# Optimization experiments

Measured on AMD Instinct MI355X. Metric: run time of the kernel, lower is better.

## Reference

```python
import jax, jax.numpy as jnp
import numpy as np

N = 50000      # num_labels (nodes)
HID = 64       # hidden_dim
HEADS = 4
CH = 16        # hidden_dim // 4 per head
R = 4          # relations
E = 200000     # edges per relation
DEPTH = 2
SLOPE = 0.2    # GATv2 leaky_relu negative slope
EPS = 1e-5     # LayerNorm eps


def layer_norm(x, g, b):
    mu = jnp.mean(x, axis=-1, keepdims=True)
    var = jnp.mean((x - mu) ** 2, axis=-1, keepdims=True)
    return (x - mu) / jnp.sqrt(var + EPS) * g + b


def setup_inputs() -> dict:
    key = jax.random.key(0)
    ks = jax.random.split(key, 8)
    # edges with src != dst (PyG remove_self_loops is then a no-op)
    src = jax.random.randint(ks[0], (R, E), 0, N, dtype=jnp.int32)
    off = jax.random.randint(ks[1], (R, E), 1, N, dtype=jnp.int32)
    dst = ((src + off) % N).astype(jnp.int32)
    edge_index = jnp.stack([src, dst], axis=1)  # [R, 2, E]
    s = 1.0 / np.sqrt(HID)
    return {
        "label_embeddings": jax.random.normal(ks[2], (N, HID), jnp.float32) * 0.5,
        "entry_w": jax.random.normal(ks[3], (HID, HID), jnp.float32) * s,
        "entry_b": jnp.zeros((HID,), jnp.float32),
        "entry_ln_g": jnp.ones((HID,), jnp.float32),
        "entry_ln_b": jnp.zeros((HID,), jnp.float32),
        "conv_wl": jax.random.normal(ks[4], (DEPTH, R, HID, HEADS * CH), jnp.float32) * s,
        "conv_wr": jax.random.normal(ks[5], (DEPTH, R, HID, HEADS * CH), jnp.float32) * s,
        "conv_att": jax.random.normal(ks[6], (DEPTH, R, HEADS, CH), jnp.float32) * (1.0 / np.sqrt(CH)),
        "conv_bias": jnp.zeros((DEPTH, R, HEADS * CH), jnp.float32),
        "norm_g": jnp.ones((HID,), jnp.float32),
        "norm_b": jnp.zeros((HID,), jnp.float32),
        "edge_index": edge_index,
    }


def _gatv2_layer(x, wl, wr, att, bias, src, dst):
    """One GATv2Conv over one relation. x:[N,HID]; returns [N, HEADS*CH]."""
    xl = (x @ wl).reshape(N, HEADS, CH)  # source transform
    xr = (x @ wr).reshape(N, HEADS, CH)  # target transform
    m = xl[src] + xr[dst]                          # [E+N, HEADS, CH]
    e = jnp.einsum('ehc,hc->eh', jax.nn.leaky_relu(m, SLOPE), att)  # [E+N, HEADS]
    # segment softmax over incoming edges of each dst node
    emax = jax.ops.segment_max(e, dst, num_segments=N)  # [N, HEADS]
    a = jnp.exp(e - emax[dst])
    denom = jax.ops.segment_sum(a, dst, num_segments=N)
    alpha = a / denom[dst]                          # every node has a self-loop -> denom > 0
    msg = xl[src] * alpha[..., None]                # [E+N, HEADS, CH]
    out = jax.ops.segment_sum(msg, dst, num_segments=N).reshape(N, HEADS * CH)
    return out + bias


def reference(label_embeddings, entry_w, entry_b, entry_ln_g, entry_ln_b,
              conv_wl, conv_wr, conv_att, conv_bias, norm_g, norm_b, edge_index):
    x = jax.nn.gelu(layer_norm(label_embeddings @ entry_w + entry_b, entry_ln_g, entry_ln_b),
                    approximate=False)
    loop = jnp.arange(N, dtype=edge_index.dtype)
    for layer in range(DEPTH):
        outs = []
        for r in range(R):
            src = jnp.concatenate([edge_index[r, 0], loop])  # add self-loops (PyG default)
            dst = jnp.concatenate([edge_index[r, 1], loop])
            outs.append(_gatv2_layer(x, conv_wl[layer, r], conv_wr[layer, r],
                                     conv_att[layer, r], conv_bias[layer, r], src, dst))
        x = sum(outs) / R                              # HeteroConv aggr='mean'
        x = layer_norm(jax.nn.gelu(x, approximate=False), norm_g, norm_b)  # dropout = identity (eval)
    return x
```

## Files before the change

### kernel.cpp

```cpp
#include <hip/hip_runtime.h>
#include <hip/hip_bf16.h>

#define NN 50000
#define RR 4
#define EE 200000
#define CAP 32

typedef __hip_bfloat16 bf16;
typedef __attribute__((ext_vector_type(8))) short short8;
typedef __attribute__((ext_vector_type(4))) float float4v;
typedef __attribute__((ext_vector_type(2))) float float2v;

__device__ __forceinline__ float b2f(bf16 v) { return __bfloat162float(v); }
__device__ __forceinline__ unsigned short f2bu(float v) {
    bf16 h = __float2bfloat16(v);
    return *(unsigned short*)&h;
}
__device__ __forceinline__ float ldf(const void* p, int i, int isbf) {
    return isbf ? __bfloat162float(((const bf16*)p)[i]) : ((const float*)p)[i];
}
__device__ __forceinline__ int dtype_isbf(const void* lg) {
    return ((const unsigned*)lg)[0] == 0x3F803F80u;
}
__device__ __forceinline__ float gelu_exact(float x) {
    return 0.5f * x * (1.0f + erff(x * 0.70710678118654752f));
}
__device__ __forceinline__ float lrelu(float m) { return fmaxf(m, 0.2f * m); }
__device__ __forceinline__ float2v bp2(unsigned u) {
    float2v f;
    f.x = __uint_as_float(u << 16);
    f.y = __uint_as_float(u & 0xffff0000u);
    return f;
}
__device__ __forceinline__ float2v lrelu2(float2v m) {
    float2v s = m * 0.2f;
    float2v r;
    r.x = fmaxf(m.x, s.x);
    r.y = fmaxf(m.y, s.y);
    return r;
}

#define PW_ENTRY_W 0
#define PW_ENTRY_B 4096
#define PW_LN_G    4160
#define PW_LN_B    4224
#define PW_WL      4288
#define PW_ATT     69824
#define PW_BIAS    70336
#define PW_NG      70848
#define PW_NB      70912
#define PW_TOT     70976

#define WT_ELEMS (2 * RR * 128 * 64)

__global__ __launch_bounds__(256) void cvt_k(const void* ew, const void* eb, const void* lg,
                                             const void* lb, const void* wl, const void* wr,
                                             const void* at, const void* bi, const void* ng,
                                             const void* nb,
                                             float* __restrict__ P, bf16* __restrict__ WT,
                                             int* __restrict__ cnt) {
    int i = blockIdx.x * 256 + threadIdx.x;
    int isbf = dtype_isbf(lg);
    if (i < RR * NN) cnt[i] = 0;
    if (i < WT_ELEMS) {
        int k = i & 63;
        int c = (i >> 6) & 127;
        int lr = i >> 13;
        float v = (c < 64) ? ldf(wl, (lr * 64 + k) * 64 + c, isbf)
                           : ldf(wr, (lr * 64 + k) * 64 + (c - 64), isbf);
        WT[i] = __float2bfloat16(v);
    }
    if (i < PW_TOT) {
        const void* src = nullptr;
        int off = 0;
        if (i < PW_ENTRY_B)      { src = ew; off = i - PW_ENTRY_W; }
        else if (i < PW_LN_G)    { src = eb; off = i - PW_ENTRY_B; }
        else if (i < PW_LN_B)    { src = lg; off = i - PW_LN_G; }
        else if (i < PW_WL)      { src = lb; off = i - PW_LN_B; }
        else if (i < PW_ATT)     { src = nullptr; }
        else if (i < PW_BIAS)    { src = at; off = i - PW_ATT; }
        else if (i < PW_NG)      { src = bi; off = i - PW_BIAS; }
        else if (i < PW_NB)      { src = ng; off = i - PW_NG; }
        else                     { src = nb; off = i - PW_NB; }
        if (src) P[i] = ldf(src, off, isbf);
    }
}

__global__ void scatter_k(const int* __restrict__ ei, int* __restrict__ cnt,
                          int* __restrict__ col) {
    int e = blockIdx.x * 256 + threadIdx.x;
    int r = blockIdx.y;
    if (e < EE) {
        int s = ei[r * 2 * EE + e];
        int d = ei[r * 2 * EE + EE + e];
        int p = atomicAdd(&cnt[r * NN + d], 1);
        if (p < CAP) col[((size_t)r * NN + d) * CAP + p] = s;
    }
}

__global__ __launch_bounds__(256) void entry_k(const void* __restrict__ emb,
                                               const void* __restrict__ lg,
                                               const float* __restrict__ P,
                                               bf16* __restrict__ xout) {
    int wave = (blockIdx.x * 256 + threadIdx.x) >> 6;
    int c = threadIdx.x & 63;
    if (wave >= NN) return;
    int isbf = dtype_isbf(lg);
    float ev = ldf(emb, wave * 64 + c, isbf);
    float acc = 0.f;
#pragma unroll 8
    for (int k = 0; k < 64; k++) {
        float xv = __shfl(ev, k, 64);
        acc += xv * P[PW_ENTRY_W + k * 64 + c];
    }
    acc += P[PW_ENTRY_B + c];
    float s = acc;
#pragma unroll
    for (int m = 1; m < 64; m <<= 1) s += __shfl_xor(s, m, 64);
    float mu = s * (1.f / 64.f);
    float d = acc - mu;
    float vs = d * d;
#pragma unroll
    for (int m = 1; m < 64; m <<= 1) vs += __shfl_xor(vs, m, 64);
    float var = vs * (1.f / 64.f);
    float y = d * rsqrtf(var + 1e-5f) * P[PW_LN_G + c] + P[PW_LN_B + c];
    xout[wave * 64 + c] = __float2bfloat16(gelu_exact(y));
}

__global__ __launch_bounds__(256) void gemm_m(const bf16* __restrict__ X,
                                              const bf16* __restrict__ WTlayer,
                                              bf16* __restrict__ xlB,
                                              bf16* __restrict__ xrB) {
    int r = blockIdx.y;
    const short* Xs = (const short*)X;
    const short* WT = (const short*)(WTlayer + (size_t)r * 8192);
    bf16* xl = xlB + (size_t)r * NN * 64;
    bf16* xr = xrB + (size_t)r * NN * 64;

    __shared__ float sh[16 * 132];
    int t = threadIdx.x;
    int w = t >> 6;
    int lane = t & 63;
    int m = lane & 15, kq = lane >> 4;
    int row0 = blockIdx.x * 16;

    const short* ap = Xs + (row0 + m) * 64 + kq * 8;
    short8 a0 = *(const short8*)ap;
    short8 a1 = *(const short8*)(ap + 32);

#pragma unroll
    for (int tile = 0; tile < 2; tile++) {
        int ct = w * 2 + tile;
        int c0 = ct * 16 + m;
        const short* bp = WT + c0 * 64 + kq * 8;
        short8 b0 = *(const short8*)bp;
        short8 b1 = *(const short8*)(bp + 32);
        float4v acc = {0.f, 0.f, 0.f, 0.f};
        asm volatile(
            "v_mfma_f32_16x16x32_bf16 %0, %1, %2, %0\n\t"
            "v_mfma_f32_16x16x32_bf16 %0, %3, %4, %0\n\t"
            "s_nop 7\n\t"
            "s_nop 7"
            : "+v"(acc)
            : "v"(a0), "v"(b0), "v"(a1), "v"(b1));
#pragma unroll
        for (int i = 0; i < 4; i++) sh[(kq * 4 + i) * 132 + c0] = acc[i];
    }
    __syncthreads();
    int row = t >> 4, cg = (t & 15) * 8;
    float v0 = sh[row * 132 + cg + 0], v1 = sh[row * 132 + cg + 1];
    float v2 = sh[row * 132 + cg + 2], v3 = sh[row * 132 + cg + 3];
    float v4 = sh[row * 132 + cg + 4], v5 = sh[row * 132 + cg + 5];
    float v6 = sh[row * 132 + cg + 6], v7 = sh[row * 132 + cg + 7];
    uint4 u;
    u.x = ((unsigned)f2bu(v1) << 16) | f2bu(v0);
    u.y = ((unsigned)f2bu(v3) << 16) | f2bu(v2);
    u.z = ((unsigned)f2bu(v5) << 16) | f2bu(v4);
    u.w = ((unsigned)f2bu(v7) << 16) | f2bu(v6);
    size_t grow = row0 + row;
    if (cg < 64) *(uint4*)&xl[grow * 64 + cg] = u;
    else         *(uint4*)&xr[grow * 64 + (cg - 64)] = u;
}

__global__ __launch_bounds__(256) void aggfin_k(const bf16* __restrict__ xlB,
                                                const bf16* __restrict__ xrB,
                                                const float* __restrict__ attL,
                                                const float* __restrict__ biasL,
                                                const int* __restrict__ cnt,
                                                const int* __restrict__ col,
                                                const float* __restrict__ P,
                                                const void* __restrict__ lg,
                                                void* __restrict__ outp,
                                                int finalOut) {
    __shared__ float shRes[RR][4][68];
    int t = threadIdx.x;
    int r = t >> 6;
    int lane = t & 63;
    int nodeBase = blockIdx.x * 4;
    int nn = lane >> 4, es = (lane >> 2) & 3, h = lane & 3;
    int node = nodeBase + nn;

    const unsigned* xl = (const unsigned*)(xlB + (size_t)r * NN * 64);
    const unsigned* xr = (const unsigned*)(xrB + (size_t)r * NN * 64);
    const float* att = attL + r * 64;
    const float* bias = biasL + r * 64;

    float2v at2[8], xr2[8];
    {
        const float4* ap = (const float4*)(att + h * 16);
#pragma unroll
        for (int i = 0; i < 4; i++) {
            float4 a = ap[i];
            at2[2 * i].x = a.x * 1.44269504f; at2[2 * i].y = a.y * 1.44269504f;
            at2[2 * i + 1].x = a.z * 1.44269504f; at2[2 * i + 1].y = a.w * 1.44269504f;
        }
        const uint4* q = (const uint4*)(xr + node * 32 + h * 8);
        uint4 u0 = q[0], u1 = q[1];
        xr2[0] = bp2(u0.x); xr2[1] = bp2(u0.y); xr2[2] = bp2(u0.z); xr2[3] = bp2(u0.w);
        xr2[4] = bp2(u1.x); xr2[5] = bp2(u1.y); xr2[6] = bp2(u1.z); xr2[7] = bp2(u1.w);
    }
    int cn = cnt[r * NN + node];
    if (cn > CAP) cn = CAP;
    int total = cn + 1;
    int kmax = total;
    kmax = max(kmax, __shfl_xor(kmax, 16, 64));
    kmax = max(kmax, __shfl_xor(kmax, 32, 64));
    const int* bucket = col + ((size_t)r * NN + node) * CAP;

    float2v A2[8];
#pragma unroll
    for (int i = 0; i < 8; i++) A2[i] = (float2v){0.f, 0.f};
    float D = 0.f;

    int k = es;
    if (k < kmax) {
        bool act = k < total;
        int src = (act && k > 0) ? bucket[k - 1] : node;
        const uint4* q = (const uint4*)(xl + src * 32 + h * 8);
        uint4 u0 = q[0], u1 = q[1];
        for (;;) {
            int kn = k + 4;
            bool more = kn < kmax;
            bool actn = false;
            uint4 n0, n1;
            if (more) {
                actn = kn < total;
                int srcn = actn ? bucket[kn - 1] : node;
                const uint4* qn = (const uint4*)(xl + srcn * 32 + h * 8);
                n0 = qn[0]; n1 = qn[1];
            }
            float2v x2[8];
            x2[0] = bp2(u0.x); x2[1] = bp2(u0.y); x2[2] = bp2(u0.z); x2[3] = bp2(u0.w);
            x2[4] = bp2(u1.x); x2[5] = bp2(u1.y); x2[6] = bp2(u1.z); x2[7] = bp2(u1.w);
            float2v t2 = (float2v){0.f, 0.f};
#pragma unroll
            for (int i = 0; i < 8; i++)
                t2 = t2 + lrelu2(x2[i] + xr2[i]) * at2[i];
            float tt = t2.x + t2.y;
            float p = act ? exp2f(tt) : 0.f;
            D += p;
            float2v p2 = (float2v){p, p};
#pragma unroll
            for (int i = 0; i < 8; i++) A2[i] = A2[i] + p2 * x2[i];
            if (!more) break;
            k = kn; act = actn; u0 = n0; u1 = n1;
        }
    }
    D += __shfl_xor(D, 4, 64);
    D += __shfl_xor(D, 8, 64);
#pragma unroll
    for (int i = 0; i < 8; i++) {
        A2[i].x += __shfl_xor(A2[i].x, 4, 64);
        A2[i].x += __shfl_xor(A2[i].x, 8, 64);
        A2[i].y += __shfl_xor(A2[i].y, 4, 64);
        A2[i].y += __shfl_xor(A2[i].y, 8, 64);
    }
    if (es == 0) {
        float inv = __builtin_amdgcn_rcpf(D);
        const float4* bp = (const float4*)(bias + h * 16);
        float* dst = &shRes[r][nn][h * 16];
#pragma unroll
        for (int i = 0; i < 4; i++) {
            float4 b = bp[i];
            dst[4 * i + 0] = A2[2 * i].x * inv + b.x;
            dst[4 * i + 1] = A2[2 * i].y * inv + b.y;
            dst[4 * i + 2] = A2[2 * i + 1].x * inv + b.z;
            dst[4 * i + 3] = A2[2 * i + 1].y * inv + b.w;
        }
    }
    __syncthreads();
    int wn = t >> 6, c = t & 63;
    float v = shRes[0][wn][c] + shRes[1][wn][c] + shRes[2][wn][c] + shRes[3][wn][c];
    v = gelu_exact(v * 0.25f);
    float s = v;
#pragma unroll
    for (int m = 1; m < 64; m <<= 1) s += __shfl_xor(s, m, 64);
    float mu = s * (1.f / 64.f);
    float d = v - mu;
    float vs = d * d;
#pragma unroll
    for (int m = 1; m < 64; m <<= 1) vs += __shfl_xor(vs, m, 64);
    float var = vs * (1.f / 64.f);
    float y = d * rsqrtf(var + 1e-5f) * P[PW_NG + c] + P[PW_NB + c];
    size_t o = (size_t)(nodeBase + wn) * 64 + c;
    if (!finalOut) {
        ((bf16*)outp)[o] = __float2bfloat16(y);
    } else {
        if (dtype_isbf(lg)) ((bf16*)outp)[o] = __float2bfloat16(y);
        else                ((float*)outp)[o] = y;
    }
}

extern "C" void kernel_launch(void* const* d_in, const int* in_sizes, int n_in,
                              void* d_out, int out_size, void* d_ws, size_t ws_size,
                              hipStream_t stream) {
    const void* emb = d_in[0];
    const void* lg  = d_in[3];
    const int*  ei  = (const int*)d_in[11];

    const size_t BUF = (size_t)NN * 64;

    bf16* X   = (bf16*)d_ws;
    bf16* XL  = X + BUF;
    bf16* XR  = XL + RR * BUF;
    bf16* WT  = XR + RR * BUF;
    float* P  = (float*)(WT + WT_ELEMS);
    int* cnt  = (int*)(P + PW_TOT);
    int* col  = cnt + RR * NN;

    int cvtN = RR * NN;
    cvt_k<<<(cvtN + 255) / 256, 256, 0, stream>>>(d_in[1], d_in[2], d_in[3], d_in[4],
                                                  d_in[5], d_in[6], d_in[7], d_in[8],
                                                  d_in[9], d_in[10], P, WT, cnt);
    scatter_k<<<dim3((EE + 255) / 256, RR), 256, 0, stream>>>(ei, cnt, col);

    int nodeBlocks = (NN + 3) / 4;
    int tileBlocks = NN / 16;

    entry_k<<<nodeBlocks, 256, 0, stream>>>(emb, lg, P, X);

    for (int l = 0; l < 2; l++) {
        gemm_m<<<dim3(tileBlocks, RR), 256, 0, stream>>>(X, WT + (size_t)l * RR * 8192, XL, XR);
        aggfin_k<<<nodeBlocks, 256, 0, stream>>>(
            XL, XR, P + PW_ATT + (size_t)l * RR * 64, P + PW_BIAS + (size_t)l * RR * 64,
            cnt, col, P, lg, (l == 0) ? (void*)X : d_out, l);
    }
}
```

Baseline: 370.7 us.

## Fuse prep kernels into one launch and remap aggregation to node-per-wave

The separate conversion, edge-scatter and entry kernels are merged into a single block-partitioned prep kernel, and the count reset moves to a memset. The entry path now reads weights straight from the inputs, so it no longer waits on the conversion pass. The aggregation kernel now gives each wave one node, with its four relations spread across lanes. Cross-relation sums use wave shuffles instead of a block-wide shared-memory reduction and __syncthreads, at the cost of 16 extra shuffle pairs per lane and a heavier, more divergent prep kernel.

```diff
diff --git a/kernel.cpp b/kernel.cpp
--- a/kernel.cpp
+++ b/kernel.cpp
@@ -11,7 +11,6 @@
 typedef __attribute__((ext_vector_type(4))) float float4v;
 typedef __attribute__((ext_vector_type(2))) float float2v;
 
-__device__ __forceinline__ float b2f(bf16 v) { return __bfloat162float(v); }
 __device__ __forceinline__ unsigned short f2bu(float v) {
     bf16 h = __float2bfloat16(v);
     return *(unsigned short*)&h;
@@ -25,7 +24,6 @@
 __device__ __forceinline__ float gelu_exact(float x) {
     return 0.5f * x * (1.0f + erff(x * 0.70710678118654752f));
 }
-__device__ __forceinline__ float lrelu(float m) { return fmaxf(m, 0.2f * m); }
 __device__ __forceinline__ float2v bp2(unsigned u) {
     float2v f;
     f.x = __uint_as_float(u << 16);
@@ -53,78 +51,76 @@
 
 #define WT_ELEMS (2 * RR * 128 * 64)
 
-__global__ __launch_bounds__(256) void cvt_k(const void* ew, const void* eb, const void* lg,
-                                             const void* lb, const void* wl, const void* wr,
-                                             const void* at, const void* bi, const void* ng,
-                                             const void* nb,
-                                             float* __restrict__ P, bf16* __restrict__ WT,
-                                             int* __restrict__ cnt) {
-    int i = blockIdx.x * 256 + threadIdx.x;
+#define ENTRY_BLKS 12500
+#define SCAT_BLKS  3125
+#define CVT_BLKS   278
+
+__global__ __launch_bounds__(256) void prep_k(const void* emb, const void* ew, const void* eb,
+                                              const void* lg, const void* lb, const void* wl,
+                                              const void* wr, const void* at, const void* bi,
+                                              const void* ng, const void* nb,
+                                              const int* __restrict__ ei,
+                                              bf16* __restrict__ X, float* __restrict__ P,
+                                              bf16* __restrict__ WT, int* __restrict__ cnt,
+                                              int* __restrict__ col) {
+    int b = blockIdx.x;
+    int t = threadIdx.x;
     int isbf = dtype_isbf(lg);
-    if (i < RR * NN) cnt[i] = 0;
-    if (i < WT_ELEMS) {
-        int k = i & 63;
-        int c = (i >> 6) & 127;
-        int lr = i >> 13;
-        float v = (c < 64) ? ldf(wl, (lr * 64 + k) * 64 + c, isbf)
-                           : ldf(wr, (lr * 64 + k) * 64 + (c - 64), isbf);
-        WT[i] = __float2bfloat16(v);
-    }
-    if (i < PW_TOT) {
-        const void* src = nullptr;
-        int off = 0;
-        if (i < PW_ENTRY_B)      { src = ew; off = i - PW_ENTRY_W; }
-        else if (i < PW_LN_G)    { src = eb; off = i - PW_ENTRY_B; }
-        else if (i < PW_LN_B)    { src = lg; off = i - PW_LN_G; }
-        else if (i < PW_WL)      { src = lb; off = i - PW_LN_B; }
-        else if (i < PW_ATT)     { src = nullptr; }
-        else if (i < PW_BIAS)    { src = at; off = i - PW_ATT; }
-        else if (i < PW_NG)      { src = bi; off = i - PW_BIAS; }
-        else if (i < PW_NB)      { src = ng; off = i - PW_NG; }
-        else                     { src = nb; off = i - PW_NB; }
-        if (src) P[i] = ldf(src, off, isbf);
-    }
-}
-
-__global__ void scatter_k(const int* __restrict__ ei, int* __restrict__ cnt,
-                          int* __restrict__ col) {
-    int e = blockIdx.x * 256 + threadIdx.x;
-    int r = blockIdx.y;
-    if (e < EE) {
+    if (b < ENTRY_BLKS) {
+        int node = b * 4 + (t >> 6);
+        int c = t & 63;
+        float ev = ldf(emb, node * 64 + c, isbf);
+        float acc = 0.f;
+#pragma unroll 8
+        for (int k = 0; k < 64; k++) {
+            float xv = __shfl(ev, k, 64);
+            acc += xv * ldf(ew, k * 64 + c, isbf);
+        }
+        acc += ldf(eb, c, isbf);
+        float s = acc;
+#pragma unroll
+        for (int m = 1; m < 64; m <<= 1) s += __shfl_xor(s, m, 64);
+        float mu = s * (1.f / 64.f);
+        float d = acc - mu;
+        float vs = d * d;
+#pragma unroll
+        for (int m = 1; m < 64; m <<= 1) vs += __shfl_xor(vs, m, 64);
+        float var = vs * (1.f / 64.f);
+        float y = d * rsqrtf(var + 1e-5f) * ldf(lg, c, isbf) + ldf(lb, c, isbf);
+        X[node * 64 + c] = __float2bfloat16(gelu_exact(y));
+    } else if (b < ENTRY_BLKS + SCAT_BLKS) {
+        int i = (b - ENTRY_BLKS) * 256 + t;
+        int r = i / EE;
+        int e = i - r * EE;
         int s = ei[r * 2 * EE + e];
         int d = ei[r * 2 * EE + EE + e];
         int p = atomicAdd(&cnt[r * NN + d], 1);
         if (p < CAP) col[((size_t)r * NN + d) * CAP + p] = s;
-    }
-}
-
-__global__ __launch_bounds__(256) void entry_k(const void* __restrict__ emb,
-                                               const void* __restrict__ lg,
-                                               const float* __restrict__ P,
-                                               bf16* __restrict__ xout) {
-    int wave = (blockIdx.x * 256 + threadIdx.x) >> 6;
-    int c = threadIdx.x & 63;
-    if (wave >= NN) return;
-    int isbf = dtype_isbf(lg);
-    float ev = ldf(emb, wave * 64 + c, isbf);
-    float acc = 0.f;
-#pragma unroll 8
-    for (int k = 0; k < 64; k++) {
-        float xv = __shfl(ev, k, 64);
-        acc += xv * P[PW_ENTRY_W + k * 64 + c];
-    }
-    acc += P[PW_ENTRY_B + c];
-    float s = acc;
-#pragma unroll
-    for (int m = 1; m < 64; m <<= 1) s += __shfl_xor(s, m, 64);
-    float mu = s * (1.f / 64.f);
-    float d = acc - mu;
-    float vs = d * d;
-#pragma unroll
-    for (int m = 1; m < 64; m <<= 1) vs += __shfl_xor(vs, m, 64);
-    float var = vs * (1.f / 64.f);
-    float y = d * rsqrtf(var + 1e-5f) * P[PW_LN_G + c] + P[PW_LN_B + c];
-    xout[wave * 64 + c] = __float2bfloat16(gelu_exact(y));
+    } else {
+        int i = (b - ENTRY_BLKS - SCAT_BLKS) * 256 + t;
+        if (i < WT_ELEMS) {
+            int k = i & 63;
+            int c = (i >> 6) & 127;
+            int lr = i >> 13;
+            float v = (c < 64) ? ldf(wl, (lr * 64 + k) * 64 + c, isbf)
+                               : ldf(wr, (lr * 64 + k) * 64 + (c - 64), isbf);
+            WT[i] = __float2bfloat16(v);
+        }
+        if (i < PW_TOT) {
+            const void* src = nullptr;
+            int off = 0;
+            if (i < PW_ENTRY_B)      { src = ew; off = i - PW_ENTRY_W; }
+            else if (i < PW_LN_G)    { src = eb; off = i - PW_ENTRY_B; }
+            else if (i < PW_LN_B)    { src = lg; off = i - PW_LN_G; }
+            else if (i < PW_WL)      { src = lb; off = i - PW_LN_B; }
+            else if (i < PW_ATT)     { src = nullptr; }
+            else if (i < PW_BIAS)    { src = at; off = i - PW_ATT; }
+            else if (i < PW_NG)      { src = bi; off = i - PW_BIAS; }
+            else if (i < PW_NB)      { src = ng; off = i - PW_NG; }
+            else                     { src = nb; off = i - PW_NB; }
+            if (src) P[i] = ldf(src, off, isbf);
+        }
+    }
 }
 
 __global__ __launch_bounds__(256) void gemm_m(const bf16* __restrict__ X,
@@ -192,22 +188,20 @@
                                                 const void* __restrict__ lg,
                                                 void* __restrict__ outp,
                                                 int finalOut) {
-    __shared__ float shRes[RR][4][68];
+    __shared__ float xp[4][72];
     int t = threadIdx.x;
-    int r = t >> 6;
-    int lane = t & 63;
-    int nodeBase = blockIdx.x * 4;
-    int nn = lane >> 4, es = (lane >> 2) & 3, h = lane & 3;
-    int node = nodeBase + nn;
-
-    const unsigned* xl = (const unsigned*)(xlB + (size_t)r * NN * 64);
-    const unsigned* xr = (const unsigned*)(xrB + (size_t)r * NN * 64);
-    const float* att = attL + r * 64;
-    const float* bias = biasL + r * 64;
+    int wv = t >> 6, lane = t & 63;
+    int node = blockIdx.x * 4 + wv;
+    int rel = lane >> 4, es = (lane >> 2) & 3, h = lane & 3;
+
+    const unsigned* xl = (const unsigned*)(xlB + (size_t)rel * NN * 64);
+    const unsigned* xr = (const unsigned*)(xrB + (size_t)rel * NN * 64);
+    const float* att = attL + rel * 64 + h * 16;
+    const float* bias = biasL + rel * 64 + h * 16;
 
     float2v at2[8], xr2[8];
     {
-        const float4* ap = (const float4*)(att + h * 16);
+        const float4* ap = (const float4*)att;
 #pragma unroll
         for (int i = 0; i < 4; i++) {
             float4 a = ap[i];
@@ -219,13 +213,13 @@
         xr2[0] = bp2(u0.x); xr2[1] = bp2(u0.y); xr2[2] = bp2(u0.z); xr2[3] = bp2(u0.w);
         xr2[4] = bp2(u1.x); xr2[5] = bp2(u1.y); xr2[6] = bp2(u1.z); xr2[7] = bp2(u1.w);
     }
-    int cn = cnt[r * NN + node];
+    int cn = cnt[rel * NN + node];
     if (cn > CAP) cn = CAP;
     int total = cn + 1;
     int kmax = total;
     kmax = max(kmax, __shfl_xor(kmax, 16, 64));
     kmax = max(kmax, __shfl_xor(kmax, 32, 64));
-    const int* bucket = col + ((size_t)r * NN + node) * CAP;
+    const int* bucket = col + ((size_t)rel * NN + node) * CAP;
 
     float2v A2[8];
 #pragma unroll
@@ -275,22 +269,32 @@
         A2[i].y += __shfl_xor(A2[i].y, 4, 64);
         A2[i].y += __shfl_xor(A2[i].y, 8, 64);
     }
-    if (es == 0) {
-        float inv = __builtin_amdgcn_rcpf(D);
-        const float4* bp = (const float4*)(bias + h * 16);
-        float* dst = &shRes[r][nn][h * 16];
+    float inv = __builtin_amdgcn_rcpf(D);
+    float res[16];
+    {
+        const float4* bp = (const float4*)bias;
 #pragma unroll
         for (int i = 0; i < 4; i++) {
             float4 b = bp[i];
-            dst[4 * i + 0] = A2[2 * i].x * inv + b.x;
-            dst[4 * i + 1] = A2[2 * i].y * inv + b.y;
-            dst[4 * i + 2] = A2[2 * i + 1].x * inv + b.z;
-            dst[4 * i + 3] = A2[2 * i + 1].y * inv + b.w;
-        }
-    }
-    __syncthreads();
-    int wn = t >> 6, c = t & 63;
-    float v = shRes[0][wn][c] + shRes[1][wn][c] + shRes[2][wn][c] + shRes[3][wn][c];
+            res[4 * i + 0] = A2[2 * i].x * inv + b.x;
+            res[4 * i + 1] = A2[2 * i].y * inv + b.y;
+            res[4 * i + 2] = A2[2 * i + 1].x * inv + b.z;
+            res[4 * i + 3] = A2[2 * i + 1].y * inv + b.w;
+        }
+    }
+#pragma unroll
+    for (int c = 0; c < 16; c++) {
+        res[c] += __shfl_xor(res[c], 16, 64);
+        res[c] += __shfl_xor(res[c], 32, 64);
+    }
+    if (lane < 4) {
+        float4* dst = (float4*)&xp[wv][lane * 16];
+        dst[0] = make_float4(res[0], res[1], res[2], res[3]);
+        dst[1] = make_float4(res[4], res[5], res[6], res[7]);
+        dst[2] = make_float4(res[8], res[9], res[10], res[11]);
+        dst[3] = make_float4(res[12], res[13], res[14], res[15]);
+    }
+    float v = xp[wv][lane];
     v = gelu_exact(v * 0.25f);
     float s = v;
 #pragma unroll
@@ -301,23 +305,18 @@
 #pragma unroll
     for (int m = 1; m < 64; m <<= 1) vs += __shfl_xor(vs, m, 64);
     float var = vs * (1.f / 64.f);
-    float y = d * rsqrtf(var + 1e-5f) * P[PW_NG + c] + P[PW_NB + c];
-    size_t o = (size_t)(nodeBase + wn) * 64 + c;
-    if (!finalOut) {
-        ((bf16*)outp)[o] = __float2bfloat16(y);
-    } else {
-        if (dtype_isbf(lg)) ((bf16*)outp)[o] = __float2bfloat16(y);
-        else                ((float*)outp)[o] = y;
-    }
+    float y = d * rsqrtf(var + 1e-5f) * P[PW_NG + lane] + P[PW_NB + lane];
+    size_t o = (size_t)node * 64 + lane;
+    int isbf = finalOut ? dtype_isbf(lg) : 1;
+    if (isbf) ((bf16*)outp)[o] = __float2bfloat16(y);
+    else      ((float*)outp)[o] = y;
 }
 
 extern "C" void kernel_launch(void* const* d_in, const int* in_sizes, int n_in,
                               void* d_out, int out_size, void* d_ws, size_t ws_size,
                               hipStream_t stream) {
-    const void* emb = d_in[0];
-    const void* lg  = d_in[3];
-    const int*  ei  = (const int*)d_in[11];
-
+    const void* lg = d_in[3];
+    const int* ei  = (const int*)d_in[11];
     const size_t BUF = (size_t)NN * 64;
 
     bf16* X   = (bf16*)d_ws;
@@ -328,16 +327,13 @@
     int* cnt  = (int*)(P + PW_TOT);
     int* col  = cnt + RR * NN;
 
-    int cvtN = RR * NN;
-    cvt_k<<<(cvtN + 255) / 256, 256, 0, stream>>>(d_in[1], d_in[2], d_in[3], d_in[4],
-                                                  d_in[5], d_in[6], d_in[7], d_in[8],
-                                                  d_in[9], d_in[10], P, WT, cnt);
-    scatter_k<<<dim3((EE + 255) / 256, RR), 256, 0, stream>>>(ei, cnt, col);
-
-    int nodeBlocks = (NN + 3) / 4;
+    hipMemsetAsync(cnt, 0, RR * NN * sizeof(int), stream);
+    prep_k<<<ENTRY_BLKS + SCAT_BLKS + CVT_BLKS, 256, 0, stream>>>(
+        d_in[0], d_in[1], d_in[2], d_in[3], d_in[4], d_in[5], d_in[6], d_in[7],
+        d_in[8], d_in[9], d_in[10], ei, X, P, WT, cnt, col);
+
     int tileBlocks = NN / 16;
-
-    entry_k<<<nodeBlocks, 256, 0, stream>>>(emb, lg, P, X);
+    int nodeBlocks = NN / 4;
 
     for (int l = 0; l < 2; l++) {
         gemm_m<<<dim3(tileBlocks, RR), 256, 0, stream>>>(X, WT + (size_t)l * RR * 8192, XL, XR);
```

Result: slower. 383.8 us (+3.5%).
